# Kernel tuning notes

Measured on AMD Instinct MI355X. Metric: run time of the kernel, lower is better.

Reference implementation:

```python
import jax, jax.numpy as jnp
import numpy as np

B, N, T, D = 32, 64, 128, 64    # batch, num_states(nodes), seq length, per-state input dim
EMB, H, E = 128, 256, 512       # emb_dim, graph_output_dim (GRU hidden), num edges


def setup_inputs() -> dict:
    key = jax.random.key(0)
    ks = jax.random.split(key, 12)
    s = 0.05
    x = jax.random.normal(ks[0], (B, N, T, D), jnp.float32)
    final_index = jax.random.randint(ks[1], (B,), 1, T + 1)
    edge_src = jax.random.randint(ks[2], (E,), 0, N)
    edge_dst = jax.random.randint(ks[3], (E,), 0, N)
    # per-node init embedding Linear (emb_init ModuleList)
    W_init = jax.random.normal(ks[4], (N, EMB, D), jnp.float32) * s
    b_init = jnp.zeros((N, EMB), jnp.float32)
    # shared GCN-style graph transform (concrete choice for opaque graph_func)
    Wg = jax.random.normal(ks[5], (EMB, H), jnp.float32) * s
    bg = jnp.zeros((H,), jnp.float32)
    # per-node GRUCell weights, torch layout: gates ordered [r, z, n]
    W_ih = jax.random.normal(ks[6], (N, 3 * H, D), jnp.float32) * s
    W_hh = jax.random.normal(ks[7], (N, 3 * H, H), jnp.float32) * s
    b_ih = jnp.zeros((N, 3 * H), jnp.float32)
    b_hh = jnp.zeros((N, 3 * H), jnp.float32)
    # per-node last_funcs: Linear(H, EMB) + Tanh
    W_last = jax.random.normal(ks[8], (N, EMB, H), jnp.float32) * s
    b_last = jnp.zeros((N, EMB), jnp.float32)
    return dict(x=x, final_index=final_index, edge_src=edge_src, edge_dst=edge_dst,
                W_init=W_init, b_init=b_init, Wg=Wg, bg=bg,
                W_ih=W_ih, W_hh=W_hh, b_ih=b_ih, b_hh=b_hh,
                W_last=W_last, b_last=b_last)


def reference(x, final_index, edge_src, edge_dst, W_init, b_init, Wg, bg,
              W_ih, W_hh, b_ih, b_hh, W_last, b_last):
    # degree with self-loops (dgl.add_self_loop)
    deg = jnp.zeros((N,), x.dtype).at[edge_dst].add(1.0) + 1.0

    def gcn(e):  # e: (B, N, EMB) -> (B, N, H); mean aggregation over in-edges + self
        agg = e + jnp.zeros_like(e).at[:, edge_dst].add(e[:, edge_src])
        agg = agg / deg[None, :, None]
        return jnp.tanh(jnp.einsum('bnf,fh->bnh', agg, Wg) + bg)

    def step(e, x_t):
        ge = gcn(e)  # (B, N, H) — hidden state fed to per-node GRUCells
        gx = jnp.einsum('bnd,ngd->bng', x_t, W_ih) + b_ih   # (B, N, 3H)
        gh = jnp.einsum('bnh,ngh->bng', ge, W_hh) + b_hh    # (B, N, 3H)
        xr, xz, xn = jnp.split(gx, 3, axis=-1)
        hr, hz, hn = jnp.split(gh, 3, axis=-1)
        r = jax.nn.sigmoid(xr + hr)
        z = jax.nn.sigmoid(xz + hz)
        n = jnp.tanh(xn + r * hn)
        h = (1.0 - z) * n + z * ge                          # GRU output (B, N, H)
        e_new = jnp.tanh(jnp.einsum('bnh,nfh->bnf', h, W_last) + b_last)  # (B, N, EMB)
        return e_new, e_new

    e0 = jnp.einsum('bnd,nfd->bnf', x[:, :, 0, :], W_init) + b_init  # emb_init
    _, last = jax.lax.scan(step, e0, jnp.moveaxis(x, 2, 0))          # (T, B, N, EMB)
    out = last[final_index - 1, jnp.arange(B)]                       # (B, N, EMB)
    return out
```

## Files before the change

kernel.cpp:

```cpp
#include <hip/hip_runtime.h>

typedef unsigned short u16;
typedef unsigned long long u64;
using s8v = __attribute__((ext_vector_type(8))) short;
using f4v = __attribute__((ext_vector_type(4))) float;

#define B_   32
#define N_   64
#define T_   128
#define D_   64
#define EMB_ 128
#define H_   256
#define E_   512
#define G3_  768

#define MFMA16(a, b, c) __builtin_amdgcn_mfma_f32_16x16x32_bf16(a, b, c, 0, 0, 0)
#define LOADC(p)    __hip_atomic_load((p), __ATOMIC_RELAXED, __HIP_MEMORY_SCOPE_AGENT)
#define STOREC(p,v) __hip_atomic_store((p), (v), __ATOMIC_RELAXED, __HIP_MEMORY_SCOPE_AGENT)

union h4u { u64 u; _Float16 h[4]; };
union s8u { s8v v; u64 q[2]; };

__device__ __forceinline__ float bf2f(u16 v) {
  union { unsigned u; float f; } x; x.u = ((unsigned)v) << 16; return x.f;
}
__device__ __forceinline__ u16 f2bf(float f) {
  union { float f; unsigned u; } x; x.f = f;
  unsigned r = x.u + 0x7fffu + ((x.u >> 16) & 1u);
  return (u16)(r >> 16);
}
__device__ __forceinline__ float ldin(const void* p, size_t i, int bf) {
  return bf ? bf2f(((const u16*)p)[i]) : ((const float*)p)[i];
}
__device__ __forceinline__ float sigm_f(float x) {
  return __builtin_amdgcn_rcpf(1.f + __expf(-x));
}
__device__ __forceinline__ float tanh_f(float x) {
  return 1.f - 2.f * __builtin_amdgcn_rcpf(1.f + __expf(2.f * x));
}

__global__ __launch_bounds__(512) __attribute__((amdgpu_waves_per_eu(2, 2)))
void ggru_kernel(
    const void* __restrict__ x, const int* __restrict__ fi,
    const int* __restrict__ esrc, const int* __restrict__ edst,
    const void* __restrict__ Winit, const void* __restrict__ binit,
    const void* __restrict__ Wg, const void* __restrict__ bg,
    const void* __restrict__ Wih, const void* __restrict__ Whh,
    const void* __restrict__ bih, const void* __restrict__ bhh,
    const void* __restrict__ Wlast, const void* __restrict__ blast,
    float* __restrict__ out, int* __restrict__ gctr,
    _Float16* __restrict__ ep)
{
  const int node = blockIdx.x >> 1;
  const int s    = blockIdx.x & 1;
  const int tid  = threadIdx.x;
  const int w    = tid >> 6;
  const int lane = tid & 63;
  const int quad = lane >> 4;
  const int c    = lane & 15;

  int* __restrict__ rdy = gctr;
  int* __restrict__ gdn = gctr + 512;

  __shared__ short sEdge[E_ + 3];
  __shared__ short sOut[E_ + 2];
  __shared__ int   sCnt, sCntO;
  __shared__ int   sFi[32];
  __shared__ __align__(16) u16 xl[32][72];
  __shared__ __align__(16) u16 aggl[32][136];
  __shared__ __align__(16) u16 gelF[32][264];
  __shared__ __align__(16) u16 hl[32][136];

  int plaus = 0;
  {
    const u16* q = (const u16*)Wg;
#pragma unroll 8
    for (int i = 0; i < 512; ++i) {
      float a = fabsf(bf2f(q[i]));
      plaus += (a > 1e-4f && a < 0.3f) ? 1 : 0;
    }
  }
  const int bf = (plaus >= 450) ? 1 : 0;

  if (tid == 0) { sCnt = 0; sCntO = 0; }
  if (tid < 32) sFi[tid] = fi[tid] - 1;
  __syncthreads();
  if (edst[tid] == node) {
    int q = atomicAdd(&sCnt, 1);
    sEdge[q] = (short)esrc[tid];
  }
  if (esrc[tid] == node) {
    int q = atomicAdd(&sCntO, 1);
    sOut[q] = (short)edst[tid];
  }
  __syncthreads();
  if (tid == 0) {
    sEdge[sCnt] = (short)node;
    sEdge[sCnt + 1] = (short)node;
    sEdge[sCnt + 2] = (short)node;
    sOut[sCntO] = (short)node;
  }
  __syncthreads();
  const int cntS = sCnt + 1;
  const int cntO = sCntO + 1;
  const float invdeg = 1.0f / (float)cntS;

  const int tA = 8 * s + w, tB = 8 * (1 - s) + w;
  s8v BgA[4], BgB[4];
#pragma unroll
  for (int kt = 0; kt < 4; ++kt) {
    s8v fa, fb;
#pragma unroll
    for (int j = 0; j < 8; ++j) {
      fa[j] = (short)f2bf(ldin(Wg, (size_t)(kt * 32 + quad * 8 + j) * H_ + 16 * tA + c, bf));
      fb[j] = (short)f2bf(ldin(Wg, (size_t)(kt * 32 + quad * 8 + j) * H_ + 16 * tB + c, bf));
    }
    BgA[kt] = fa; BgB[kt] = fb;
  }
  const int hcol = 128 * s + 16 * w + c;
  s8v Bih_[3][2], Bhh_[3][8];
#pragma unroll
  for (int gt = 0; gt < 3; ++gt) {
    const size_t bih_base = (size_t)node * G3_ * D_ + (size_t)(gt * H_ + hcol) * D_;
    const size_t bhh_base = (size_t)node * G3_ * H_ + (size_t)(gt * H_ + hcol) * H_;
#pragma unroll
    for (int kt = 0; kt < 2; ++kt) {
      s8v f;
#pragma unroll
      for (int j = 0; j < 8; ++j)
        f[j] = (short)f2bf(ldin(Wih, bih_base + kt * 32 + quad * 8 + j, bf));
      Bih_[gt][kt] = f;
    }
#pragma unroll
    for (int kt = 0; kt < 8; ++kt) {
      s8v f;
#pragma unroll
      for (int j = 0; j < 8; ++j)
        f[j] = (short)f2bf(ldin(Whh, bhh_base + kt * 32 + quad * 8 + j, bf));
      Bhh_[gt][kt] = f;
    }
  }
  const int ecol = 16 * w + c;
  s8v Bl_[4];
  {
    const size_t bl_base = (size_t)node * EMB_ * H_ + (size_t)ecol * H_ + 128 * s;
#pragma unroll
    for (int kt = 0; kt < 4; ++kt) {
      s8v f;
#pragma unroll
      for (int j = 0; j < 8; ++j)
        f[j] = (short)f2bf(ldin(Wlast, bl_base + kt * 32 + quad * 8 + j, bf));
      Bl_[kt] = f;
    }
  }
  const float bgcA = ldin(bg, 16 * tA + c, bf);
  const float bgcB = ldin(bg, 16 * tB + c, bf);
  float bihv[3], bhhv[3];
#pragma unroll
  for (int gt = 0; gt < 3; ++gt) {
    bihv[gt] = ldin(bih, (size_t)node * G3_ + gt * H_ + hcol, bf);
    bhhv[gt] = ldin(bhh, (size_t)node * G3_ + gt * H_ + hcol, bf);
  }
  const float blc = (s == 0) ? ldin(blast, (size_t)node * EMB_ + ecol, bf) : 0.f;

  const size_t NODE_SZ = (size_t)B_ * EMB_;
  u64* __restrict__ epq = (u64*)ep;

  {
    const int row = tid >> 4, d0 = (tid & 15) * 4;
#pragma unroll
    for (int k = 0; k < 4; ++k)
      xl[row][d0 + k] = f2bf(ldin(x, ((size_t)row * N_ + node) * (T_ * D_) + d0 + k, bf));
  }
  __syncthreads();
  {
    const int row = tid >> 4, f0 = (tid & 15) * 8;
    u64* dst = epq + ((((size_t)(s * 4 + 0) * N_ + node) * NODE_SZ + row * EMB_ + f0) >> 2);
    if (s == 0) {
      h4u o0, o1;
#pragma unroll
      for (int ff = 0; ff < 8; ++ff) {
        const int f = f0 + ff;
        float acc = ldin(binit, (size_t)node * EMB_ + f, bf);
        const size_t wb = ((size_t)node * EMB_ + f) * D_;
#pragma unroll 8
        for (int d = 0; d < D_; ++d) acc += bf2f(xl[row][d]) * ldin(Winit, wb + d, bf);
        if (ff < 4) o0.h[ff] = (_Float16)acc; else o1.h[ff - 4] = (_Float16)acc;
      }
      STOREC(dst, o0.u); STOREC(dst + 1, o1.u);
    } else {
      STOREC(dst, 0ull); STOREC(dst + 1, 0ull);
    }
  }
  __syncthreads();
  if (tid == 0)
    STOREC(&rdy[node * 8 + s * 4], 1);

  f4v gxa[2][3];
#pragma unroll
  for (int rh = 0; rh < 2; ++rh)
#pragma unroll
    for (int g = 0; g < 3; ++g) gxa[rh][g] = (f4v){0.f, 0.f, 0.f, 0.f};
#pragma unroll
  for (int rh = 0; rh < 2; ++rh)
#pragma unroll
    for (int kt = 0; kt < 2; ++kt) {
      s8v a = *(const s8v*)&xl[16 * rh + c][kt * 32 + quad * 8];
      gxa[rh][0] = MFMA16(a, Bih_[0][kt], gxa[rh][0]);
      gxa[rh][1] = MFMA16(a, Bih_[1][kt], gxa[rh][1]);
      gxa[rh][2] = MFMA16(a, Bih_[2][kt], gxa[rh][2]);
    }

#pragma unroll 1
  for (int t = 0; t <= T_; ++t) {
    {
      const int tgt = t + 1;
      if (w == 0) {
        for (;;) {
          int ok = 1;
          for (int i = lane; i < cntS; i += 64) {
            const int m = (int)sEdge[i];
            if (LOADC(&rdy[m * 8]) < tgt || LOADC(&rdy[m * 8 + 4]) < tgt) ok = 0;
          }
          if (__all(ok)) break;
          __builtin_amdgcn_s_sleep(1);
        }
      }
      __syncthreads();
    }
    const int par = t & 3;

    if (s == 0 && t >= 1) {
      const int row = tid >> 4, f0 = (tid & 15) * 8;
      if (sFi[row] == t - 1) {
        const u64* p0 = epq + ((((size_t)(0 * 4 + par) * N_ + node) * NODE_SZ + row * EMB_ + f0) >> 2);
        const u64* p1 = epq + ((((size_t)(1 * 4 + par) * N_ + node) * NODE_SZ + row * EMB_ + f0) >> 2);
        h4u a0, a1, b0, b1;
        a0.u = LOADC((u64*)p0); a1.u = LOADC((u64*)p0 + 1);
        b0.u = LOADC((u64*)p1); b1.u = LOADC((u64*)p1 + 1);
#pragma unroll
        for (int k = 0; k < 4; ++k) {
          out[(size_t)row * (N_ * EMB_) + node * EMB_ + f0 + k] =
              tanh_f((float)a0.h[k] + (float)b0.h[k]);
          out[(size_t)row * (N_ * EMB_) + node * EMB_ + f0 + 4 + k] =
              tanh_f((float)a1.h[k] + (float)b1.h[k]);
        }
      }
    }
    if (t == T_) break;

    if (t + 1 < T_) {
      const int row = tid >> 4, d0 = (tid & 15) * 4;
#pragma unroll
      for (int k = 0; k < 4; ++k)
        xl[row][d0 + k] = f2bf(ldin(x, ((size_t)row * N_ + node) * (T_ * D_) + (size_t)(t + 1) * D_ + d0 + k, bf));
    }
    {
      const int row = tid >> 4, f0 = (tid & 15) * 8;
      u64* b0 = epq + ((((size_t)(0 * 4 + par) * N_) * NODE_SZ + row * EMB_ + f0) >> 2);
      u64* b1 = epq + ((((size_t)(1 * 4 + par) * N_) * NODE_SZ + row * EMB_ + f0) >> 2);
      float acc[8];
#pragma unroll
      for (int k = 0; k < 8; ++k) acc[k] = 0.f;
      size_t sa = (size_t)(int)sEdge[0] * (NODE_SZ >> 2);
      size_t sb = (size_t)(int)sEdge[1] * (NODE_SZ >> 2);
      u64 Aa0 = LOADC(b0 + sa), Aa1 = LOADC(b0 + sa + 1);
      u64 Ca0 = LOADC(b1 + sa), Ca1 = LOADC(b1 + sa + 1);
      u64 Ab0 = LOADC(b0 + sb), Ab1 = LOADC(b0 + sb + 1);
      u64 Cb0 = LOADC(b1 + sb), Cb1 = LOADC(b1 + sb + 1);
      if (t == 0) {
#pragma unroll 1
        for (int i = 0; i < cntS; ++i) {
          size_t sn = (size_t)(int)sEdge[i + 2] * (NODE_SZ >> 2);
          u64 nA0 = LOADC(b0 + sn), nA1 = LOADC(b0 + sn + 1);
          u64 nC0 = LOADC(b1 + sn), nC1 = LOADC(b1 + sn + 1);
          h4u a0, a1, c0, c1; a0.u = Aa0; a1.u = Aa1; c0.u = Ca0; c1.u = Ca1;
#pragma unroll
          for (int k = 0; k < 4; ++k) {
            acc[k]     += (float)a0.h[k] + (float)c0.h[k];
            acc[4 + k] += (float)a1.h[k] + (float)c1.h[k];
          }
          Aa0 = Ab0; Aa1 = Ab1; Ca0 = Cb0; Ca1 = Cb1;
          Ab0 = nA0; Ab1 = nA1; Cb0 = nC0; Cb1 = nC1;
        }
      } else {
#pragma unroll 1
        for (int i = 0; i < cntS; ++i) {
          size_t sn = (size_t)(int)sEdge[i + 2] * (NODE_SZ >> 2);
          u64 nA0 = LOADC(b0 + sn), nA1 = LOADC(b0 + sn + 1);
          u64 nC0 = LOADC(b1 + sn), nC1 = LOADC(b1 + sn + 1);
          h4u a0, a1, c0, c1; a0.u = Aa0; a1.u = Aa1; c0.u = Ca0; c1.u = Ca1;
#pragma unroll
          for (int k = 0; k < 4; ++k) {
            acc[k]     += tanh_f((float)a0.h[k] + (float)c0.h[k]);
            acc[4 + k] += tanh_f((float)a1.h[k] + (float)c1.h[k]);
          }
          Aa0 = Ab0; Aa1 = Ab1; Ca0 = Cb0; Ca1 = Cb1;
          Ab0 = nA0; Ab1 = nA1; Cb0 = nC0; Cb1 = nC1;
        }
      }
      s8v pk;
#pragma unroll
      for (int k = 0; k < 8; ++k) pk[k] = (short)f2bf(acc[k] * invdeg);
      *(s8v*)&aggl[row][f0] = pk;
    }
    __syncthreads();
    if (tid == 0)
      STOREC(&gdn[node * 8 + s * 4], t + 1);

    float gevA[2][4];
#pragma unroll
    for (int rh = 0; rh < 2; ++rh) {
      s8v a[4];
#pragma unroll
      for (int kt = 0; kt < 4; ++kt) a[kt] = *(const s8v*)&aggl[16 * rh + c][kt * 32 + quad * 8];
      f4v accA = {0.f, 0.f, 0.f, 0.f}, accB = {0.f, 0.f, 0.f, 0.f};
#pragma unroll
      for (int kt = 0; kt < 4; ++kt) {
        accA = MFMA16(a[kt], BgA[kt], accA);
        accB = MFMA16(a[kt], BgB[kt], accB);
      }
#pragma unroll
      for (int i = 0; i < 4; ++i) {
        float vA = tanh_f(accA[i] + bgcA);
        float vB = tanh_f(accB[i] + bgcB);
        gevA[rh][i] = vA;
        gelF[16 * rh + quad * 4 + i][16 * tA + c] = f2bf(vA);
        gelF[16 * rh + quad * 4 + i][16 * tB + c] = f2bf(vB);
      }
    }
    __syncthreads();

#pragma unroll
    for (int rh = 0; rh < 2; ++rh) {
      f4v aR = gxa[rh][0], aZ = gxa[rh][1], aXn = gxa[rh][2];
      f4v aHn = {0.f, 0.f, 0.f, 0.f};
#pragma unroll
      for (int kt = 0; kt < 8; ++kt) {
        s8v a = *(const s8v*)&gelF[16 * rh + c][kt * 32 + quad * 8];
        aR  = MFMA16(a, Bhh_[0][kt], aR);
        aZ  = MFMA16(a, Bhh_[1][kt], aZ);
        aHn = MFMA16(a, Bhh_[2][kt], aHn);
      }
#pragma unroll
      for (int i = 0; i < 4; ++i) {
        float r_ = sigm_f(aR[i] + bihv[0] + bhhv[0]);
        float z_ = sigm_f(aZ[i] + bihv[1] + bhhv[1]);
        float ng = tanh_f(aXn[i] + bihv[2] + r_ * (aHn[i] + bhhv[2]));
        float h  = (1.f - z_) * ng + z_ * gevA[rh][i];
        hl[16 * rh + quad * 4 + i][16 * w + c] = f2bf(h);
      }
    }
    __syncthreads();

#pragma unroll
    for (int rh = 0; rh < 2; ++rh) {
      f4v aE = {0.f, 0.f, 0.f, 0.f};
#pragma unroll
      for (int kt = 0; kt < 4; ++kt) {
        s8v a = *(const s8v*)&hl[16 * rh + c][kt * 32 + quad * 8];
        aE = MFMA16(a, Bl_[kt], aE);
      }
#pragma unroll
      for (int i = 0; i < 4; ++i) {
        const int row = 16 * rh + quad * 4 + i;
        union { _Float16 h; u16 u; } cv;
        cv.h = (_Float16)(aE[i] + blc);
        aggl[row][ecol] = cv.u;
      }
    }
    if (w == 0 && t >= 3) {
      const int tgt = t - 2;
      for (;;) {
        int ok = 1;
        for (int i = lane; i < cntO; i += 64) {
          const int m = (int)sOut[i];
          if (LOADC(&gdn[m * 8]) < tgt || LOADC(&gdn[m * 8 + 4]) < tgt) ok = 0;
        }
        if (__all(ok)) break;
        __builtin_amdgcn_s_sleep(2);
      }
    }
    __syncthreads();
    {
      const int row = tid >> 4, f0 = (tid & 15) * 8;
      s8u cv; cv.v = *(const s8v*)&aggl[row][f0];
      u64* eo = epq + ((((size_t)(s * 4 + ((t + 1) & 3)) * N_ + node) * NODE_SZ + row * EMB_ + f0) >> 2);
      STOREC(eo, cv.q[0]); STOREC(eo + 1, cv.q[1]);
    }
    __syncthreads();
    if (tid == 0)
      STOREC(&rdy[node * 8 + s * 4], t + 2);

    if (t + 1 < T_) {
#pragma unroll
      for (int rh = 0; rh < 2; ++rh) {
#pragma unroll
        for (int g = 0; g < 3; ++g) gxa[rh][g] = (f4v){0.f, 0.f, 0.f, 0.f};
#pragma unroll
        for (int kt = 0; kt < 2; ++kt) {
          s8v a = *(const s8v*)&xl[16 * rh + c][kt * 32 + quad * 8];
          gxa[rh][0] = MFMA16(a, Bih_[0][kt], gxa[rh][0]);
          gxa[rh][1] = MFMA16(a, Bih_[1][kt], gxa[rh][1]);
          gxa[rh][2] = MFMA16(a, Bih_[2][kt], gxa[rh][2]);
        }
      }
    }
  }
}

extern "C" void kernel_launch(void* const* d_in, const int* in_sizes, int n_in,
                              void* d_out, int out_size, void* d_ws, size_t ws_size,
                              hipStream_t stream) {
  const void* x     = d_in[0];
  const int*  fi    = (const int*)d_in[1];
  const int*  esrc  = (const int*)d_in[2];
  const int*  edst  = (const int*)d_in[3];
  const void* Winit = d_in[4];
  const void* binit = d_in[5];
  const void* Wg    = d_in[6];
  const void* bg    = d_in[7];
  const void* Wih   = d_in[8];
  const void* Whh   = d_in[9];
  const void* bih   = d_in[10];
  const void* bhh   = d_in[11];
  const void* Wlast = d_in[12];
  const void* blast = d_in[13];

  int*      gctr = (int*)d_ws;
  _Float16* ep   = (_Float16*)((char*)d_ws + 4096);
  hipMemsetAsync(d_ws, 0, 4096, stream);

  ggru_kernel<<<128, 512, 0, stream>>>(
      x, fi, esrc, edst, Winit, binit, Wg, bg, Wih, Whh, bih, bhh,
      Wlast, blast, (float*)d_out, gctr, ep);
}
```

Measured before the change: 2.061 ms.

## Gate neighbor gathers per-edge instead of waiting for all neighbors

Replaces the per-step barrier that waited until every in-neighbor block published its step with a per-neighbor gate. Wave 0 spins on each neighbor's ready flag and then publishes a shared-memory counter, while the other waves spin on that counter before loading that neighbor's embedding. This lets aggregation start as soon as the first neighbors are ready, overlapping the wait with work. The cost is extra spin traffic on LDS with sleep(0), and a serialized gate per edge.

```diff
diff --git a/kernel.cpp b/kernel.cpp
--- a/kernel.cpp
+++ b/kernel.cpp
@@ -66,6 +66,7 @@
   __shared__ short sOut[E_ + 2];
   __shared__ int   sCnt, sCntO;
   __shared__ int   sFi[32];
+  __shared__ int   sReadyCnt;
   __shared__ __align__(16) u16 xl[32][72];
   __shared__ __align__(16) u16 aggl[32][136];
   __shared__ __align__(16) u16 gelF[32][264];
@@ -82,6 +83,8 @@
   }
   const int bf = (plaus >= 450) ? 1 : 0;
 
+  sEdge[tid] = 0;
+  if (tid < 3) sEdge[E_ + tid] = 0;
   if (tid == 0) { sCnt = 0; sCntO = 0; }
   if (tid < 32) sFi[tid] = fi[tid] - 1;
   __syncthreads();
@@ -211,24 +214,122 @@
       gxa[rh][2] = MFMA16(a, Bih_[2][kt], gxa[rh][2]);
     }
 
+#define GATE(j)                                                              \
+  if ((j) < cntS) {                                                          \
+    if (w == 0) {                                                            \
+      const int gm = (int)sEdge[(j)];                                        \
+      for (;;) {                                                             \
+        int ok = (LOADC(&rdy[gm * 8]) >= t + 1) &&                           \
+                 (LOADC(&rdy[gm * 8 + 4]) >= t + 1);                         \
+        if (__all(ok)) break;                                                \
+        __builtin_amdgcn_s_sleep(0);                                         \
+      }                                                                      \
+      if (lane == 0) *(volatile int*)&sReadyCnt = (j) + 1;                   \
+    } else {                                                                 \
+      while (*(volatile int*)&sReadyCnt <= (j)) __builtin_amdgcn_s_sleep(0); \
+    }                                                                        \
+  }
+
 #pragma unroll 1
   for (int t = 0; t <= T_; ++t) {
-    {
-      const int tgt = t + 1;
+    if (t == T_) {
       if (w == 0) {
+        const int tgt = T_ + 1;
         for (;;) {
-          int ok = 1;
-          for (int i = lane; i < cntS; i += 64) {
-            const int m = (int)sEdge[i];
-            if (LOADC(&rdy[m * 8]) < tgt || LOADC(&rdy[m * 8 + 4]) < tgt) ok = 0;
-          }
+          int ok = (LOADC(&rdy[node * 8]) >= tgt) &&
+                   (LOADC(&rdy[node * 8 + 4]) >= tgt);
           if (__all(ok)) break;
           __builtin_amdgcn_s_sleep(1);
         }
       }
       __syncthreads();
-    }
+      if (s == 0) {
+        const int par = t & 3;
+        const int row = tid >> 4, f0 = (tid & 15) * 8;
+        if (sFi[row] == t - 1) {
+          const u64* p0 = epq + ((((size_t)(0 * 4 + par) * N_ + node) * NODE_SZ + row * EMB_ + f0) >> 2);
+          const u64* p1 = epq + ((((size_t)(1 * 4 + par) * N_ + node) * NODE_SZ + row * EMB_ + f0) >> 2);
+          h4u a0, a1, b0, b1;
+          a0.u = LOADC((u64*)p0); a1.u = LOADC((u64*)p0 + 1);
+          b0.u = LOADC((u64*)p1); b1.u = LOADC((u64*)p1 + 1);
+#pragma unroll
+          for (int k = 0; k < 4; ++k) {
+            out[(size_t)row * (N_ * EMB_) + node * EMB_ + f0 + k] =
+                tanh_f((float)a0.h[k] + (float)b0.h[k]);
+            out[(size_t)row * (N_ * EMB_) + node * EMB_ + f0 + 4 + k] =
+                tanh_f((float)a1.h[k] + (float)b1.h[k]);
+          }
+        }
+      }
+      break;
+    }
+
+    if (tid == 0) *(volatile int*)&sReadyCnt = 0;
+    __syncthreads();
     const int par = t & 3;
+
+    if (t + 1 < T_) {
+      const int row = tid >> 4, d0 = (tid & 15) * 4;
+#pragma unroll
+      for (int k = 0; k < 4; ++k)
+        xl[row][d0 + k] = f2bf(ldin(x, ((size_t)row * N_ + node) * (T_ * D_) + (size_t)(t + 1) * D_ + d0 + k, bf));
+    }
+    {
+      const int row = tid >> 4, f0 = (tid & 15) * 8;
+      u64* b0 = epq + ((((size_t)(0 * 4 + par) * N_) * NODE_SZ + row * EMB_ + f0) >> 2);
+      u64* b1 = epq + ((((size_t)(1 * 4 + par) * N_) * NODE_SZ + row * EMB_ + f0) >> 2);
+      float acc[8];
+#pragma unroll
+      for (int k = 0; k < 8; ++k) acc[k] = 0.f;
+      GATE(0)
+      size_t sa = (size_t)(int)sEdge[0] * (NODE_SZ >> 2);
+      u64 A0 = LOADC(b0 + sa), A1 = LOADC(b0 + sa + 1);
+      u64 C0 = LOADC(b1 + sa), C1 = LOADC(b1 + sa + 1);
+      GATE(1)
+      size_t sb = (size_t)(int)sEdge[1] * (NODE_SZ >> 2);
+      u64 Ab0 = LOADC(b0 + sb), Ab1 = LOADC(b0 + sb + 1);
+      u64 Cb0 = LOADC(b1 + sb), Cb1 = LOADC(b1 + sb + 1);
+      if (t == 0) {
+#pragma unroll 1
+        for (int i = 0; i < cntS; ++i) {
+          GATE(i + 2)
+          size_t sn = (size_t)(int)sEdge[i + 2] * (NODE_SZ >> 2);
+          u64 nA0 = LOADC(b0 + sn), nA1 = LOADC(b0 + sn + 1);
+          u64 nC0 = LOADC(b1 + sn), nC1 = LOADC(b1 + sn + 1);
+          h4u a0, a1, c0, c1; a0.u = A0; a1.u = A1; c0.u = C0; c1.u = C1;
+#pragma unroll
+          for (int k = 0; k < 4; ++k) {
+            acc[k]     += (float)a0.h[k] + (float)c0.h[k];
+            acc[4 + k] += (float)a1.h[k] + (float)c1.h[k];
+          }
+          A0 = Ab0; A1 = Ab1; C0 = Cb0; C1 = Cb1;
+          Ab0 = nA0; Ab1 = nA1; Cb0 = nC0; Cb1 = nC1;
+        }
+      } else {
+#pragma unroll 1
+        for (int i = 0; i < cntS; ++i) {
+          GATE(i + 2)
+          size_t sn = (size_t)(int)sEdge[i + 2] * (NODE_SZ >> 2);
+          u64 nA0 = LOADC(b0 + sn), nA1 = LOADC(b0 + sn + 1);
+          u64 nC0 = LOADC(b1 + sn), nC1 = LOADC(b1 + sn + 1);
+          h4u a0, a1, c0, c1; a0.u = A0; a1.u = A1; c0.u = C0; c1.u = C1;
+#pragma unroll
+          for (int k = 0; k < 4; ++k) {
+            acc[k]     += tanh_f((float)a0.h[k] + (float)c0.h[k]);
+            acc[4 + k] += tanh_f((float)a1.h[k] + (float)c1.h[k]);
+          }
+          A0 = Ab0; A1 = Ab1; C0 = Cb0; C1 = Cb1;
+          Ab0 = nA0; Ab1 = nA1; Cb0 = nC0; Cb1 = nC1;
+        }
+      }
+      s8v pk;
+#pragma unroll
+      for (int k = 0; k < 8; ++k) pk[k] = (short)f2bf(acc[k] * invdeg);
+      *(s8v*)&aggl[row][f0] = pk;
+    }
+    __syncthreads();
+    if (tid == 0)
+      STOREC(&gdn[node * 8 + s * 4], t + 1);
 
     if (s == 0 && t >= 1) {
       const int row = tid >> 4, f0 = (tid & 15) * 8;
@@ -247,66 +348,6 @@
         }
       }
     }
-    if (t == T_) break;
-
-    if (t + 1 < T_) {
-      const int row = tid >> 4, d0 = (tid & 15) * 4;
-#pragma unroll
-      for (int k = 0; k < 4; ++k)
-        xl[row][d0 + k] = f2bf(ldin(x, ((size_t)row * N_ + node) * (T_ * D_) + (size_t)(t + 1) * D_ + d0 + k, bf));
-    }
-    {
-      const int row = tid >> 4, f0 = (tid & 15) * 8;
-      u64* b0 = epq + ((((size_t)(0 * 4 + par) * N_) * NODE_SZ + row * EMB_ + f0) >> 2);
-      u64* b1 = epq + ((((size_t)(1 * 4 + par) * N_) * NODE_SZ + row * EMB_ + f0) >> 2);
-      float acc[8];
-#pragma unroll
-      for (int k = 0; k < 8; ++k) acc[k] = 0.f;
-      size_t sa = (size_t)(int)sEdge[0] * (NODE_SZ >> 2);
-      size_t sb = (size_t)(int)sEdge[1] * (NODE_SZ >> 2);
-      u64 Aa0 = LOADC(b0 + sa), Aa1 = LOADC(b0 + sa + 1);
-      u64 Ca0 = LOADC(b1 + sa), Ca1 = LOADC(b1 + sa + 1);
-      u64 Ab0 = LOADC(b0 + sb), Ab1 = LOADC(b0 + sb + 1);
-      u64 Cb0 = LOADC(b1 + sb), Cb1 = LOADC(b1 + sb + 1);
-      if (t == 0) {
-#pragma unroll 1
-        for (int i = 0; i < cntS; ++i) {
-          size_t sn = (size_t)(int)sEdge[i + 2] * (NODE_SZ >> 2);
-          u64 nA0 = LOADC(b0 + sn), nA1 = LOADC(b0 + sn + 1);
-          u64 nC0 = LOADC(b1 + sn), nC1 = LOADC(b1 + sn + 1);
-          h4u a0, a1, c0, c1; a0.u = Aa0; a1.u = Aa1; c0.u = Ca0; c1.u = Ca1;
-#pragma unroll
-          for (int k = 0; k < 4; ++k) {
-            acc[k]     += (float)a0.h[k] + (float)c0.h[k];
-            acc[4 + k] += (float)a1.h[k] + (float)c1.h[k];
-          }
-          Aa0 = Ab0; Aa1 = Ab1; Ca0 = Cb0; Ca1 = Cb1;
-          Ab0 = nA0; Ab1 = nA1; Cb0 = nC0; Cb1 = nC1;
-        }
-      } else {
-#pragma unroll 1
-        for (int i = 0; i < cntS; ++i) {
-          size_t sn = (size_t)(int)sEdge[i + 2] * (NODE_SZ >> 2);
-          u64 nA0 = LOADC(b0 + sn), nA1 = LOADC(b0 + sn + 1);
-          u64 nC0 = LOADC(b1 + sn), nC1 = LOADC(b1 + sn + 1);
-          h4u a0, a1, c0, c1; a0.u = Aa0; a1.u = Aa1; c0.u = Ca0; c1.u = Ca1;
-#pragma unroll
-          for (int k = 0; k < 4; ++k) {
-            acc[k]     += tanh_f((float)a0.h[k] + (float)c0.h[k]);
-            acc[4 + k] += tanh_f((float)a1.h[k] + (float)c1.h[k]);
-          }
-          Aa0 = Ab0; Aa1 = Ab1; Ca0 = Cb0; Ca1 = Cb1;
-          Ab0 = nA0; Ab1 = nA1; Cb0 = nC0; Cb1 = nC1;
-        }
-      }
-      s8v pk;
-#pragma unroll
-      for (int k = 0; k < 8; ++k) pk[k] = (short)f2bf(acc[k] * invdeg);
-      *(s8v*)&aggl[row][f0] = pk;
-    }
-    __syncthreads();
-    if (tid == 0)
-      STOREC(&gdn[node * 8 + s * 4], t + 1);
 
     float gevA[2][4];
 #pragma unroll
@@ -407,6 +448,7 @@
       }
     }
   }
+#undef GATE
 }
 
 extern "C" void kernel_launch(void* const* d_in, const int* in_sizes, int n_in,
```

Result: slower. 2.526 ms (+22.5%).
